# Optimization experiments

Hardware: AMD Instinct MI355X
Metric: run time of the kernel (lower is better)

The kernel has to match this reference:

```python
import jax, jax.numpy as jnp
import numpy as np

N = 16384
DIMS = [3, 256, 256, 256, 256, 256, 256, 3]
NU = 1.0 / 100.0  # 1 / Reynold


def setup_inputs() -> dict:
    key = jax.random.key(0)
    ks = jax.random.split(key, 3 + 2 * (len(DIMS) - 1))
    inp = {
        "t": jax.random.uniform(ks[0], (N, 1), dtype=jnp.float32),
        "x": jax.random.uniform(ks[1], (N, 1), dtype=jnp.float32),
        "y": jax.random.uniform(ks[2], (N, 1), dtype=jnp.float32),
    }
    for i in range(len(DIMS) - 1):
        fan_in, fan_out = DIMS[i], DIMS[i + 1]
        # glorot_normal scale
        scale = jnp.sqrt(2.0 / (fan_in + fan_out)).astype(jnp.float32)
        inp[f"W{i}"] = jax.random.normal(ks[3 + 2 * i], (fan_in, fan_out), dtype=jnp.float32) * scale
        inp[f"b{i}"] = jax.random.normal(ks[4 + 2 * i], (fan_out,), dtype=jnp.float32) * 0.01
    return inp


def _mlp(p, params):
    # p: [3] single (t,x,y) point -> [3] (u,v,p)
    h = p
    for W, b in params[:-1]:
        h = jnp.sin(h @ W + b)
    W, b = params[-1]
    return h @ W + b


def reference(t, x, y, W0, b0, W1, b1, W2, b2, W3, b3, W4, b4, W5, b5, W6, b6):
    params = [(W0, b0), (W1, b1), (W2, b2), (W3, b3), (W4, b4), (W5, b5), (W6, b6)]
    f = lambda p: _mlp(p, params)
    txy = jnp.concatenate([t, x, y], axis=1)  # [N, 3]

    uvp = jax.vmap(f)(txy)                          # [N, 3]
    J = jax.vmap(jax.jacfwd(f))(txy)                # [N, 3(out), 3(in)]
    H = jax.vmap(jax.jacfwd(jax.jacfwd(f)))(txy)    # [N, 3(out), 3(in), 3(in)]

    u, v = uvp[:, 0], uvp[:, 1]
    u_t, u_x, u_y = J[:, 0, 0], J[:, 0, 1], J[:, 0, 2]
    v_t, v_x, v_y = J[:, 1, 0], J[:, 1, 1], J[:, 1, 2]
    p_x, p_y = J[:, 2, 1], J[:, 2, 2]
    u_xx, u_yy = H[:, 0, 1, 1], H[:, 0, 2, 2]
    v_xx, v_yy = H[:, 1, 1, 1], H[:, 1, 2, 2]

    eq1 = u_t + (u * u_x + v * u_y) + p_x - NU * (u_xx + u_yy)
    eq2 = v_t + (u * v_x + v * v_y) + p_y - NU * (v_xx + v_yy)
    eq3 = u_x + v_y
    return eq1[:, None], eq2[:, None], eq3[:, None]
```

## Files before the change

### kernel.cpp

```cpp
#include <hip/hip_runtime.h>

#define NPTS 16384
#define PW 16
#define NCH 5
#define NU (1.0f / 100.0f)

typedef _Float16 f16;
typedef __attribute__((ext_vector_type(4))) _Float16 f16x4;
typedef __attribute__((ext_vector_type(8))) _Float16 f16x8;
typedef __attribute__((ext_vector_type(4))) float f32x4;

__device__ __forceinline__ int swz(int g) { return g ^ ((g >> 3) & 7); }

__global__ __launch_bounds__(256) void prep_kernel(
    const float* __restrict__ W1, const float* __restrict__ W2,
    const float* __restrict__ W3, const float* __restrict__ W4,
    const float* __restrict__ W5, const float* __restrict__ W6,
    f16* __restrict__ bh, f16* __restrict__ b6h)
{
    int idx = blockIdx.x * 256 + threadIdx.x;
    if (idx < 40960) {
        int col = idx & 255, subk = (idx >> 8) & 3, kc = (idx >> 10) & 7, L = idx >> 13;
        const float* W = (L == 0) ? W1 : (L == 1) ? W2 : (L == 2) ? W3 : (L == 3) ? W4 : W5;
        f16x8 vh;
        #pragma unroll
        for (int j = 0; j < 8; ++j) {
            int k = kc * 32 + subk * 8 + j;
            vh[j] = (f16)W[k * 256 + col];
        }
        int nf = col >> 4, l15 = col & 15, lane = subk * 16 + l15;
        *(f16x8*)(bh + (((L * 8 + kc) * 16 + nf) * 64 + lane) * 8) = vh;
    } else {
        int u = idx - 40960;
        if (u < 512) {
            int col = u & 15, subk = (u >> 4) & 3, kc = u >> 6;
            f16x8 vh;
            #pragma unroll
            for (int j = 0; j < 8; ++j) {
                int k = kc * 32 + subk * 8 + j;
                vh[j] = (f16)((col < 3) ? W6[k * 3 + col] : 0.f);
            }
            *(f16x8*)(b6h + (kc * 64 + subk * 16 + col) * 8) = vh;
        }
    }
}

__global__ __launch_bounds__(256) void pinn_ns_mfma(
    const float* __restrict__ t_, const float* __restrict__ x_, const float* __restrict__ y_,
    const float* __restrict__ W0, const float* __restrict__ b0,
    const float* __restrict__ b1, const float* __restrict__ b2,
    const float* __restrict__ b3, const float* __restrict__ b4,
    const float* __restrict__ b5, const float* __restrict__ b6,
    const f16* __restrict__ bh, const f16* __restrict__ b6h,
    float* __restrict__ out)
{
    __shared__ __align__(16) f16 afrag[NCH * 8 * 512];

    const int tid = threadIdx.x;
    const int lane = tid & 63;
    const int nq = tid >> 6;
    const int q = lane >> 4;
    const int s = lane & 15;
    const int gl = swz(lane);
    const int p0 = blockIdx.x * PW;

    {
        float tv = t_[p0 + s], xv = x_[p0 + s], yv = y_[p0 + s];
        int fq0 = tid >> 4;
        #pragma unroll
        for (int i = 0; i < 4; ++i) {
            int fq = fq0 + 16 * i;
            int f0 = fq * 4;
            f32x4 w0 = *(const f32x4*)&W0[f0];
            f32x4 w1 = *(const f32x4*)&W0[256 + f0];
            f32x4 w2 = *(const f32x4*)&W0[512 + f0];
            f32x4 bb = *(const f32x4*)&b0[f0];
            f16x4 o[NCH];
            #pragma unroll
            for (int ff = 0; ff < 4; ++ff) {
                float z = tv * w0[ff] + xv * w1[ff] + yv * w2[ff] + bb[ff];
                float sv, cv;
                __sincosf(z, &sv, &cv);
                o[0][ff] = (f16)sv;
                o[1][ff] = (f16)(cv * w0[ff]);
                o[2][ff] = (f16)(cv * w1[ff]);
                o[3][ff] = (f16)(cv * w2[ff]);
                o[4][ff] = (f16)(-sv * (w1[ff] * w1[ff] + w2[ff] * w2[ff]));
            }
            int kc = fq >> 3;
            int g = swz(16 * ((fq >> 1) & 3) + s);
            int half = fq & 1;
            #pragma unroll
            for (int c = 0; c < NCH; ++c)
                *(f16x4*)&afrag[(c * 8 + kc) * 512 + g * 8 + half * 4] = o[c];
        }
    }
    __syncthreads();

    const float* bias[5] = {b1, b2, b3, b4, b5};
    const f16x8* A = (const f16x8*)afrag;
    for (int L = 0; L < 5; ++L) {
        const f16x8* wH = (const f16x8*)bh + L * 8192;
        f32x4 acc[NCH][4];
        #pragma unroll
        for (int c = 0; c < NCH; ++c)
            #pragma unroll
            for (int f = 0; f < 4; ++f)
                acc[c][f] = (f32x4){0.f, 0.f, 0.f, 0.f};

        f16x8 Wc[4];
        #pragma unroll
        for (int f = 0; f < 4; ++f)
            Wc[f] = wH[(nq * 4 + f) * 64 + lane];

        #pragma unroll
        for (int kc = 0; kc < 8; ++kc) {
            f16x8 Wn[4];
            if (kc < 7) {
                #pragma unroll
                for (int f = 0; f < 4; ++f)
                    Wn[f] = wH[((kc + 1) * 16 + nq * 4 + f) * 64 + lane];
            }
            f16x8 S[NCH];
            #pragma unroll
            for (int c = 0; c < NCH; ++c)
                S[c] = A[(c * 8 + kc) * 64 + gl];
            #pragma unroll
            for (int c = 0; c < NCH; ++c)
                #pragma unroll
                for (int f = 0; f < 4; ++f)
                    acc[c][f] = __builtin_amdgcn_mfma_f32_16x16x32_f16(Wc[f], S[c], acc[c][f], 0, 0, 0);
            if (kc < 7) {
                #pragma unroll
                for (int f = 0; f < 4; ++f)
                    Wc[f] = Wn[f];
            }
        }
        __syncthreads();

        const float* bbp = bias[L];
        #pragma unroll
        for (int mf = 0; mf < 4; ++mf) {
            int fbase = nq * 64 + mf * 16 + 4 * q;
            f32x4 bq = *(const f32x4*)&bbp[fbase];
            f16x4 o[NCH];
            #pragma unroll
            for (int r = 0; r < 4; ++r) {
                float z = acc[0][mf][r] + bq[r];
                float zt = acc[1][mf][r], zx = acc[2][mf][r], zy = acc[3][mf][r];
                float zlap = acc[4][mf][r];
                float sv, cv;
                __sincosf(z, &sv, &cv);
                o[0][r] = (f16)sv;
                o[1][r] = (f16)(cv * zt);
                o[2][r] = (f16)(cv * zx);
                o[3][r] = (f16)(cv * zy);
                o[4][r] = (f16)(cv * zlap - sv * (zx * zx + zy * zy));
            }
            int kc = 2 * nq + (mf >> 1);
            int g = swz(16 * (2 * (mf & 1) + (q >> 1)) + s);
            int half = q & 1;
            #pragma unroll
            for (int c = 0; c < NCH; ++c)
                *(f16x4*)&afrag[(c * 8 + kc) * 512 + g * 8 + half * 4] = o[c];
        }
        __syncthreads();
    }

    if (nq == 0) {
        f32x4 a6[NCH];
        #pragma unroll
        for (int c = 0; c < NCH; ++c)
            a6[c] = (f32x4){0.f, 0.f, 0.f, 0.f};
        const f16x8* w6 = (const f16x8*)b6h;
        #pragma unroll
        for (int kc = 0; kc < 8; ++kc) {
            f16x8 Wf = w6[kc * 64 + lane];
            #pragma unroll
            for (int c = 0; c < NCH; ++c)
                a6[c] = __builtin_amdgcn_mfma_f32_16x16x32_f16(Wf, A[(c * 8 + kc) * 64 + gl], a6[c], 0, 0, 0);
        }
        if (lane < 16) {
            int g = p0 + s;
            float u_   = a6[0][0] + b6[0], v_ = a6[0][1] + b6[1];
            float ut   = a6[1][0], vt   = a6[1][1];
            float ux   = a6[2][0], vx   = a6[2][1], px = a6[2][2];
            float uy   = a6[3][0], vy   = a6[3][1], py = a6[3][2];
            float ulap = a6[4][0], vlap = a6[4][1];
            out[g]            = ut + (u_ * ux + v_ * uy) + px - NU * ulap;
            out[NPTS + g]     = vt + (u_ * vx + v_ * vy) + py - NU * vlap;
            out[2 * NPTS + g] = ux + vy;
        }
    }
}

extern "C" void kernel_launch(void* const* d_in, const int* in_sizes, int n_in,
                              void* d_out, int out_size, void* d_ws, size_t ws_size,
                              hipStream_t stream) {
    const float* t_ = (const float*)d_in[0];
    const float* x_ = (const float*)d_in[1];
    const float* y_ = (const float*)d_in[2];
    const float* W[7];
    const float* b[7];
    for (int i = 0; i < 7; ++i) {
        W[i] = (const float*)d_in[3 + 2 * i];
        b[i] = (const float*)d_in[4 + 2 * i];
    }
    float* out = (float*)d_out;

    f16* bh  = (f16*)d_ws;
    f16* b6h = bh + 5 * 65536;

    hipLaunchKernelGGL(prep_kernel, dim3(162), dim3(256), 0, stream,
                       W[1], W[2], W[3], W[4], W[5], W[6], bh, b6h);
    hipLaunchKernelGGL(pinn_ns_mfma, dim3(NPTS / PW), dim3(256), 0, stream,
                       t_, x_, y_, W[0], b[0],
                       b[1], b[2], b[3], b[4], b[5], b[6],
                       bh, b6h, out);
}
```

Measured before the change: 143.8 us.

## Process two point groups per block, interleaving MFMA and sine activations

Each block now handles two 16-point groups held in separate LDS buffers, with the tensor-core matmul of one group interleaved against the sin/cos activation of the other. The goal is to overlap MFMA and transcendental work and halve the number of barrier-separated phases per point. The final 3-wide layer is spread across all four waves and reduced through LDS. The cost is doubled LDS use and two accumulator sets live at once, which raises register pressure and may lower occupancy. Weight prefetching was also dropped from the inner loop.

```diff
diff --git a/kernel.cpp b/kernel.cpp
--- a/kernel.cpp
+++ b/kernel.cpp
@@ -4,6 +4,7 @@
 #define PW 16
 #define NCH 5
 #define NU (1.0f / 100.0f)
+#define JETELEMS (NCH * 8 * 512)
 
 typedef _Float16 f16;
 typedef __attribute__((ext_vector_type(4))) _Float16 f16x4;
@@ -43,6 +44,112 @@
             *(f16x8*)(b6h + (kc * 64 + subk * 16 + col) * 8) = vh;
         }
     }
+}
+
+
+__device__ __forceinline__ void mfma_layer(const f16x8* __restrict__ wH,
+                                           const f16* __restrict__ stJ,
+                                           int lane, int nq, int gl,
+                                           f32x4 (&acc)[NCH][4])
+{
+    #pragma unroll
+    for (int c = 0; c < NCH; ++c)
+        #pragma unroll
+        for (int f = 0; f < 4; ++f)
+            acc[c][f] = (f32x4){0.f, 0.f, 0.f, 0.f};
+    const f16x8* AJ = (const f16x8*)stJ;
+    #pragma unroll
+    for (int kc = 0; kc < 8; ++kc) {
+        f16x8 Wc[4];
+        #pragma unroll
+        for (int f = 0; f < 4; ++f)
+            Wc[f] = wH[(kc * 16 + nq * 4 + f) * 64 + lane];
+        f16x8 S[NCH];
+        #pragma unroll
+        for (int c = 0; c < NCH; ++c)
+            S[c] = AJ[(c * 8 + kc) * 64 + gl];
+        #pragma unroll
+        for (int c = 0; c < NCH; ++c)
+            #pragma unroll
+            for (int f = 0; f < 4; ++f)
+                acc[c][f] = __builtin_amdgcn_mfma_f32_16x16x32_f16(Wc[f], S[c], acc[c][f], 0, 0, 0);
+    }
+}
+
+__device__ __forceinline__ void act_layer(const float* __restrict__ bbp,
+                                          f16* __restrict__ stJ,
+                                          int nq, int q, int s,
+                                          f32x4 (&acc)[NCH][4])
+{
+    #pragma unroll
+    for (int mf = 0; mf < 4; ++mf) {
+        int fbase = nq * 64 + mf * 16 + 4 * q;
+        f32x4 bq = *(const f32x4*)&bbp[fbase];
+        f16x4 o[NCH];
+        #pragma unroll
+        for (int r = 0; r < 4; ++r) {
+            float z = acc[0][mf][r] + bq[r];
+            float zt = acc[1][mf][r], zx = acc[2][mf][r], zy = acc[3][mf][r];
+            float zlap = acc[4][mf][r];
+            float sv = __sinf(z), cv = __cosf(z);
+            o[0][r] = (f16)sv;
+            o[1][r] = (f16)(cv * zt);
+            o[2][r] = (f16)(cv * zx);
+            o[3][r] = (f16)(cv * zy);
+            o[4][r] = (f16)(cv * zlap - sv * (zx * zx + zy * zy));
+        }
+        int kc = 2 * nq + (mf >> 1);
+        int g = swz(16 * (2 * (mf & 1) + (q >> 1)) + s);
+        int half = q & 1;
+        #pragma unroll
+        for (int c = 0; c < NCH; ++c)
+            *(f16x4*)&stJ[(c * 8 + kc) * 512 + g * 8 + half * 4] = o[c];
+    }
+}
+
+__device__ __forceinline__ void layer0(const float* __restrict__ W0,
+                                       const float* __restrict__ b0,
+                                       float tv, float xv, float yv,
+                                       f16* __restrict__ stJ, int tid, int s)
+{
+    int fq0 = tid >> 4;
+    #pragma unroll
+    for (int i = 0; i < 4; ++i) {
+        int fq = fq0 + 16 * i;
+        int f0 = fq * 4;
+        f32x4 w0 = *(const f32x4*)&W0[f0];
+        f32x4 w1 = *(const f32x4*)&W0[256 + f0];
+        f32x4 w2 = *(const f32x4*)&W0[512 + f0];
+        f32x4 bb = *(const f32x4*)&b0[f0];
+        f16x4 o[NCH];
+        #pragma unroll
+        for (int ff = 0; ff < 4; ++ff) {
+            float z = tv * w0[ff] + xv * w1[ff] + yv * w2[ff] + bb[ff];
+            float sv = __sinf(z), cv = __cosf(z);
+            o[0][ff] = (f16)sv;
+            o[1][ff] = (f16)(cv * w0[ff]);
+            o[2][ff] = (f16)(cv * w1[ff]);
+            o[3][ff] = (f16)(cv * w2[ff]);
+            o[4][ff] = (f16)(-sv * (w1[ff] * w1[ff] + w2[ff] * w2[ff]));
+        }
+        int kc = fq >> 3;
+        int g = swz(16 * ((fq >> 1) & 3) + s);
+        int half = fq & 1;
+        #pragma unroll
+        for (int c = 0; c < NCH; ++c)
+            *(f16x4*)&stJ[(c * 8 + kc) * 512 + g * 8 + half * 4] = o[c];
+    }
+}
+
+__device__ __forceinline__ void mfma6(const f16* __restrict__ stJ,
+                                      const f16x8* __restrict__ w6,
+                                      int lane, int gl, int c, f32x4& a6)
+{
+    a6 = (f32x4){0.f, 0.f, 0.f, 0.f};
+    const f16x8* AJ = (const f16x8*)stJ;
+    #pragma unroll
+    for (int kc = 0; kc < 8; ++kc)
+        a6 = __builtin_amdgcn_mfma_f32_16x16x32_f16(w6[kc * 64 + lane], AJ[(c * 8 + kc) * 64 + gl], a6, 0, 0, 0);
 }
 
 __global__ __launch_bounds__(256) void pinn_ns_mfma(
@@ -54,7 +161,7 @@
     const f16* __restrict__ bh, const f16* __restrict__ b6h,
     float* __restrict__ out)
 {
-    __shared__ __align__(16) f16 afrag[NCH * 8 * 512];
+    __shared__ __align__(16) f16 afrag[2 * JETELEMS];
 
     const int tid = threadIdx.x;
     const int lane = tid & 63;
@@ -62,135 +169,87 @@
     const int q = lane >> 4;
     const int s = lane & 15;
     const int gl = swz(lane);
-    const int p0 = blockIdx.x * PW;
-
-    {
-        float tv = t_[p0 + s], xv = x_[p0 + s], yv = y_[p0 + s];
-        int fq0 = tid >> 4;
-        #pragma unroll
-        for (int i = 0; i < 4; ++i) {
-            int fq = fq0 + 16 * i;
-            int f0 = fq * 4;
-            f32x4 w0 = *(const f32x4*)&W0[f0];
-            f32x4 w1 = *(const f32x4*)&W0[256 + f0];
-            f32x4 w2 = *(const f32x4*)&W0[512 + f0];
-            f32x4 bb = *(const f32x4*)&b0[f0];
-            f16x4 o[NCH];
-            #pragma unroll
-            for (int ff = 0; ff < 4; ++ff) {
-                float z = tv * w0[ff] + xv * w1[ff] + yv * w2[ff] + bb[ff];
-                float sv, cv;
-                __sincosf(z, &sv, &cv);
-                o[0][ff] = (f16)sv;
-                o[1][ff] = (f16)(cv * w0[ff]);
-                o[2][ff] = (f16)(cv * w1[ff]);
-                o[3][ff] = (f16)(cv * w2[ff]);
-                o[4][ff] = (f16)(-sv * (w1[ff] * w1[ff] + w2[ff] * w2[ff]));
-            }
-            int kc = fq >> 3;
-            int g = swz(16 * ((fq >> 1) & 3) + s);
-            int half = fq & 1;
-            #pragma unroll
-            for (int c = 0; c < NCH; ++c)
-                *(f16x4*)&afrag[(c * 8 + kc) * 512 + g * 8 + half * 4] = o[c];
-        }
-    }
-    __syncthreads();
-
+    const int p0 = blockIdx.x * (2 * PW);
+
+    f16* st0 = afrag;
+    f16* st1 = afrag + JETELEMS;
+
+    layer0(W0, b0, t_[p0 + s], x_[p0 + s], y_[p0 + s], st0, tid, s);
+    layer0(W0, b0, t_[p0 + PW + s], x_[p0 + PW + s], y_[p0 + PW + s], st1, tid, s);
+    __syncthreads();
+
+    f32x4 accA[NCH][4], accB[NCH][4];
+    const f16x8* wbase = (const f16x8*)bh;
     const float* bias[5] = {b1, b2, b3, b4, b5};
-    const f16x8* A = (const f16x8*)afrag;
-    for (int L = 0; L < 5; ++L) {
-        const f16x8* wH = (const f16x8*)bh + L * 8192;
-        f32x4 acc[NCH][4];
-        #pragma unroll
-        for (int c = 0; c < NCH; ++c)
-            #pragma unroll
-            for (int f = 0; f < 4; ++f)
-                acc[c][f] = (f32x4){0.f, 0.f, 0.f, 0.f};
-
-        f16x8 Wc[4];
-        #pragma unroll
-        for (int f = 0; f < 4; ++f)
-            Wc[f] = wH[(nq * 4 + f) * 64 + lane];
-
-        #pragma unroll
-        for (int kc = 0; kc < 8; ++kc) {
-            f16x8 Wn[4];
-            if (kc < 7) {
-                #pragma unroll
-                for (int f = 0; f < 4; ++f)
-                    Wn[f] = wH[((kc + 1) * 16 + nq * 4 + f) * 64 + lane];
-            }
-            f16x8 S[NCH];
-            #pragma unroll
-            for (int c = 0; c < NCH; ++c)
-                S[c] = A[(c * 8 + kc) * 64 + gl];
-            #pragma unroll
-            for (int c = 0; c < NCH; ++c)
-                #pragma unroll
-                for (int f = 0; f < 4; ++f)
-                    acc[c][f] = __builtin_amdgcn_mfma_f32_16x16x32_f16(Wc[f], S[c], acc[c][f], 0, 0, 0);
-            if (kc < 7) {
-                #pragma unroll
-                for (int f = 0; f < 4; ++f)
-                    Wc[f] = Wn[f];
-            }
-        }
+
+    mfma_layer(wbase, st0, lane, nq, gl, accA);
+    __syncthreads();
+
+    for (int i = 1; i <= 4; ++i) {
+        const f16x8* wI  = wbase + (i - 1) * 8192;
+        const f16x8* wI1 = wbase + i * 8192;
+        const float* bi = bias[i - 1];
+        mfma_layer(wI, st1, lane, nq, gl, accB);
+        act_layer(bi, st0, nq, q, s, accA);
         __syncthreads();
-
-        const float* bbp = bias[L];
-        #pragma unroll
-        for (int mf = 0; mf < 4; ++mf) {
-            int fbase = nq * 64 + mf * 16 + 4 * q;
-            f32x4 bq = *(const f32x4*)&bbp[fbase];
-            f16x4 o[NCH];
-            #pragma unroll
-            for (int r = 0; r < 4; ++r) {
-                float z = acc[0][mf][r] + bq[r];
-                float zt = acc[1][mf][r], zx = acc[2][mf][r], zy = acc[3][mf][r];
-                float zlap = acc[4][mf][r];
-                float sv, cv;
-                __sincosf(z, &sv, &cv);
-                o[0][r] = (f16)sv;
-                o[1][r] = (f16)(cv * zt);
-                o[2][r] = (f16)(cv * zx);
-                o[3][r] = (f16)(cv * zy);
-                o[4][r] = (f16)(cv * zlap - sv * (zx * zx + zy * zy));
-            }
-            int kc = 2 * nq + (mf >> 1);
-            int g = swz(16 * (2 * (mf & 1) + (q >> 1)) + s);
-            int half = q & 1;
-            #pragma unroll
-            for (int c = 0; c < NCH; ++c)
-                *(f16x4*)&afrag[(c * 8 + kc) * 512 + g * 8 + half * 4] = o[c];
-        }
+        mfma_layer(wI1, st0, lane, nq, gl, accA);
+        act_layer(bi, st1, nq, q, s, accB);
         __syncthreads();
     }
 
-    if (nq == 0) {
-        f32x4 a6[NCH];
-        #pragma unroll
-        for (int c = 0; c < NCH; ++c)
-            a6[c] = (f32x4){0.f, 0.f, 0.f, 0.f};
-        const f16x8* w6 = (const f16x8*)b6h;
-        #pragma unroll
-        for (int kc = 0; kc < 8; ++kc) {
-            f16x8 Wf = w6[kc * 64 + lane];
-            #pragma unroll
-            for (int c = 0; c < NCH; ++c)
-                a6[c] = __builtin_amdgcn_mfma_f32_16x16x32_f16(Wf, A[(c * 8 + kc) * 64 + gl], a6[c], 0, 0, 0);
-        }
-        if (lane < 16) {
-            int g = p0 + s;
-            float u_   = a6[0][0] + b6[0], v_ = a6[0][1] + b6[1];
-            float ut   = a6[1][0], vt   = a6[1][1];
-            float ux   = a6[2][0], vx   = a6[2][1], px = a6[2][2];
-            float uy   = a6[3][0], vy   = a6[3][1], py = a6[3][2];
-            float ulap = a6[4][0], vlap = a6[4][1];
-            out[g]            = ut + (u_ * ux + v_ * uy) + px - NU * ulap;
-            out[NPTS + g]     = vt + (u_ * vx + v_ * vy) + py - NU * vlap;
-            out[2 * NPTS + g] = ux + vy;
-        }
+    const f16x8* w5 = wbase + 4 * 8192;
+    const f16x8* w6 = (const f16x8*)b6h;
+
+    mfma_layer(w5, st1, lane, nq, gl, accB);
+    act_layer(b5, st0, nq, q, s, accA);
+    __syncthreads();
+
+    f32x4 a6m, a6l;
+    mfma6(st0, w6, lane, gl, nq, a6m);
+    if (nq == 0) mfma6(st0, w6, lane, gl, 4, a6l);
+    act_layer(b5, st1, nq, q, s, accB);
+    __syncthreads();
+
+    float* z0 = (float*)st0;
+    if (q == 0) {
+        #pragma unroll
+        for (int r = 0; r < 3; ++r)
+            z0[(nq * 3 + r) * 16 + s] = a6m[r] + (nq == 0 ? b6[r] : 0.f);
+        if (nq == 0) {
+            #pragma unroll
+            for (int r = 0; r < 3; ++r)
+                z0[(12 + r) * 16 + s] = a6l[r];
+        }
+    }
+    mfma6(st1, w6, lane, gl, nq, a6m);
+    if (nq == 0) mfma6(st1, w6, lane, gl, 4, a6l);
+    __syncthreads();
+
+    float* z1 = (float*)st1;
+    if (q == 0) {
+        #pragma unroll
+        for (int r = 0; r < 3; ++r)
+            z1[(nq * 3 + r) * 16 + s] = a6m[r] + (nq == 0 ? b6[r] : 0.f);
+        if (nq == 0) {
+            #pragma unroll
+            for (int r = 0; r < 3; ++r)
+                z1[(12 + r) * 16 + s] = a6l[r];
+        }
+    }
+    __syncthreads();
+
+    if (tid < 32) {
+        int j = tid >> 4, ss = tid & 15;
+        const float* zJ = (const float*)(afrag + j * JETELEMS);
+        float u_   = zJ[0 * 16 + ss],  v_   = zJ[1 * 16 + ss];
+        float ut   = zJ[3 * 16 + ss],  vt   = zJ[4 * 16 + ss];
+        float ux   = zJ[6 * 16 + ss],  vx   = zJ[7 * 16 + ss],  px = zJ[8 * 16 + ss];
+        float uy   = zJ[9 * 16 + ss],  vy   = zJ[10 * 16 + ss], py = zJ[11 * 16 + ss];
+        float ulap = zJ[12 * 16 + ss], vlap = zJ[13 * 16 + ss];
+        int g = p0 + j * PW + ss;
+        out[g]            = ut + (u_ * ux + v_ * uy) + px - NU * ulap;
+        out[NPTS + g]     = vt + (u_ * vx + v_ * vy) + py - NU * vlap;
+        out[2 * NPTS + g] = ux + vy;
     }
 }
 
@@ -213,7 +272,7 @@
 
     hipLaunchKernelGGL(prep_kernel, dim3(162), dim3(256), 0, stream,
                        W[1], W[2], W[3], W[4], W[5], W[6], bh, b6h);
-    hipLaunchKernelGGL(pinn_ns_mfma, dim3(NPTS / PW), dim3(256), 0, stream,
+    hipLaunchKernelGGL(pinn_ns_mfma, dim3(NPTS / (2 * PW)), dim3(256), 0, stream,
                        t_, x_, y_, W[0], b[0],
                        b[1], b[2], b[3], b[4], b[5], b[6],
                        bh, b6h, out);
```

After: 156.0 us. 8.5% more time.
